# Kernel optimization log

Measured on AMD Instinct MI355X. Metric: run time of the kernel, lower is better.

## Reference

```python
import jax, jax.numpy as jnp
import numpy as np

TOP_K = 2

def setup_inputs() -> dict:
    key = jax.random.key(0)
    k1, k2 = jax.random.split(key)
    T, D, E = 16384, 2048, 64  # num_tokens, d_model, num_experts
    x = jax.random.normal(k1, (T, D), dtype=jnp.float32)
    Wg = jax.random.normal(k2, (D, E), dtype=jnp.float32) / np.sqrt(D)
    return {"x": x, "Wg": Wg}

def reference(x, Wg):
    T, E = x.shape[0], Wg.shape[1]
    # gate logits + softmax over experts
    logits = x @ Wg                                   # [T, E]
    probs = jax.nn.softmax(logits, axis=-1)           # [T, E]
    # top-k expert selection, renormalize selected weights
    top_vals, top_idx = jax.lax.top_k(probs, TOP_K)   # [T, K]
    top_vals = top_vals / jnp.sum(top_vals, axis=-1, keepdims=True)
    # scatter sparse gate weights into dense [T, E]
    rows = jnp.arange(T)[:, None]                     # [T, 1]
    gate_weights = jnp.zeros_like(probs).at[rows, top_idx].set(top_vals)
    # load-balance aux loss: E * sum_e f_e * P_e
    mask = jnp.sum(jax.nn.one_hot(top_idx, E, dtype=probs.dtype), axis=1)  # [T, E]
    f = jnp.mean(mask, axis=0)    # fraction of tokens routed to each expert
    P = jnp.mean(probs, axis=0)   # mean router prob per expert
    aux_loss = E * jnp.sum(f * P)
    return gate_weights, top_idx, aux_loss
```

## Files before the change

kernel.cpp:

```cpp
#include <hip/hip_runtime.h>


typedef __attribute__((ext_vector_type(8))) _Float16 half8;
typedef __attribute__((ext_vector_type(4))) float f32x4;

constexpr int DD  = 2048;
constexpr int EE  = 64;
constexpr int BM  = 16;
constexpr int BK  = 128;
constexpr int NCH = DD / BK;

#define WVM(N) asm volatile("s_waitcnt vmcnt(" #N ")" ::: "memory")
#define BAR()  asm volatile("s_barrier" ::: "memory")

__global__ __launch_bounds__(256) void wsplit_kernel(
    const float* __restrict__ Wg, _Float16* __restrict__ wF)
{
    __shared__ float xl[32][65];
    const int tid = threadIdx.x;
    const int kc  = blockIdx.x;
    const int k0  = kc * 32;
#pragma unroll
    for (int r = 0; r < 2; ++r) {
        int slot = tid + r * 256;
        int row = slot >> 4, c4 = (slot & 15) << 2;
        *(float4*)&xl[row][c4] = *(const float4*)&Wg[(size_t)(k0 + row) * EE + c4];
    }
    __syncthreads();
    const int t = tid >> 6, l = tid & 63;
    const int e  = t * 16 + (l & 15);
    const int kl = (l >> 4) * 8;
    half8 hh, ll;
#pragma unroll
    for (int j = 0; j < 8; ++j) {
        float v = xl[kl + j][e];
        _Float16 h = (_Float16)v;
        hh[j] = h;
        ll[j] = (_Float16)((v - (float)h) * 4096.f);
    }
    const size_t base = (size_t)(kc * 8 + t * 2) * 512 + (size_t)l * 8;
    *(half8*)&wF[base]       = hh;
    *(half8*)&wF[base + 512] = ll;
}

__global__ __launch_bounds__(256, 4) void gate_kernel(
    const float* __restrict__ x, const _Float16* __restrict__ wF,
    float* __restrict__ gate_out, float* __restrict__ idx_out,
    float* __restrict__ pSum, float* __restrict__ pCnt)
{
    __shared__ __align__(16) union {
        float xs[3][BM][BK];
        struct { float red[4][BM][68]; float auxsm[2][4][64]; } ep;
    } sm;

    const int tid  = threadIdx.x;
    const int kq   = tid >> 6;
    const int lane = tid & 63;
    const size_t tok0 = (size_t)blockIdx.x * BM;
    const float* xg = x + tok0 * DD;

    auto stageX = [&](int buf, int c) {
#pragma unroll
        for (int r = 0; r < 2; ++r) {
            int slot = tid + r * 256;
            int row  = slot >> 5;
            int cb   = (slot & 31) << 4;
            int sb   = cb ^ ((row & 7) << 5);
            __builtin_amdgcn_global_load_lds(
                xg + (size_t)row * DD + c * BK + (sb >> 2),
                &sm.xs[buf][row][cb >> 2], 16, 0, 0);
        }
    };

    f32x4 aH[4], aL[4];
#pragma unroll
    for (int t = 0; t < 4; ++t) {
        aH[t] = (f32x4){0.f, 0.f, 0.f, 0.f};
        aL[t] = (f32x4){0.f, 0.f, 0.f, 0.f};
    }

    const int rrow = lane & 15;
    const int rb   = (kq * 128 + ((lane >> 4) * 32)) ^ ((rrow & 7) << 5);

    auto compute = [&](int buf, int c) {
        const _Float16* wb = wF + (size_t)(c * 4 + kq) * 4096 + (size_t)lane * 8;
        half8 wh[4], wl[4];
#pragma unroll
        for (int t = 0; t < 4; ++t) {
            wh[t] = *(const half8*)(wb + (t * 2) * 512);
            wl[t] = *(const half8*)(wb + (t * 2 + 1) * 512);
        }
        const float* p = (const float*)((const char*)&sm.xs[buf][rrow][0] + rb);
        float4 xa = *(const float4*)p;
        float4 xb = *(const float4*)(p + 4);
        half8 ah, al;
        {
            float v;
            v = xa.x; { _Float16 h=(_Float16)v; ah[0]=h; al[0]=(_Float16)((v-(float)h)*4096.f); }
            v = xa.y; { _Float16 h=(_Float16)v; ah[1]=h; al[1]=(_Float16)((v-(float)h)*4096.f); }
            v = xa.z; { _Float16 h=(_Float16)v; ah[2]=h; al[2]=(_Float16)((v-(float)h)*4096.f); }
            v = xa.w; { _Float16 h=(_Float16)v; ah[3]=h; al[3]=(_Float16)((v-(float)h)*4096.f); }
            v = xb.x; { _Float16 h=(_Float16)v; ah[4]=h; al[4]=(_Float16)((v-(float)h)*4096.f); }
            v = xb.y; { _Float16 h=(_Float16)v; ah[5]=h; al[5]=(_Float16)((v-(float)h)*4096.f); }
            v = xb.z; { _Float16 h=(_Float16)v; ah[6]=h; al[6]=(_Float16)((v-(float)h)*4096.f); }
            v = xb.w; { _Float16 h=(_Float16)v; ah[7]=h; al[7]=(_Float16)((v-(float)h)*4096.f); }
        }
#pragma unroll
        for (int t = 0; t < 4; ++t) {
            aH[t] = __builtin_amdgcn_mfma_f32_16x16x32_f16(ah, wh[t], aH[t], 0, 0, 0);
            aL[t] = __builtin_amdgcn_mfma_f32_16x16x32_f16(ah, wl[t], aL[t], 0, 0, 0);
            aL[t] = __builtin_amdgcn_mfma_f32_16x16x32_f16(al, wh[t], aL[t], 0, 0, 0);
        }
    };

    stageX(0, 0);
    stageX(1, 1);

#pragma unroll 1
    for (int c = 0; c < NCH; ++c) {
        if (c < NCH - 1) { WVM(2); } else { WVM(0); }
        BAR();
        compute(c % 3, c);
        BAR();
        if (c + 2 < NCH) stageX((c + 2) % 3, c + 2);
    }

    __syncthreads();
    const float inv = 1.f / 4096.f;
#pragma unroll
    for (int e = 0; e < 4; ++e) {
        const int row = (lane >> 4) * 4 + e;
#pragma unroll
        for (int t = 0; t < 4; ++t)
            sm.ep.red[kq][row][t * 16 + (lane & 15)] = aH[t][e] + aL[t][e] * inv;
    }
    __syncthreads();

    float sumP_acc = 0.f;
    float cnt_acc  = 0.f;
#pragma unroll 1
    for (int tt = 0; tt < 4; ++tt) {
        const int tl = kq * 4 + tt;
        const size_t t = tok0 + tl;
        float v = (sm.ep.red[0][tl][lane] + sm.ep.red[1][tl][lane])
                + (sm.ep.red[2][tl][lane] + sm.ep.red[3][tl][lane]);

        float m = v;
#pragma unroll
        for (int off = 32; off; off >>= 1) m = fmaxf(m, __shfl_xor(m, off, 64));
        float p = expf(v - m);
        float s = p;
#pragma unroll
        for (int off = 32; off; off >>= 1) s += __shfl_xor(s, off, 64);
        float prob = p / s;
        sumP_acc += prob;

        float bv = prob; int bi = lane;
#pragma unroll
        for (int off = 32; off; off >>= 1) {
            float ov = __shfl_xor(bv, off, 64);
            int   oi = __shfl_xor(bi, off, 64);
            if (ov > bv || (ov == bv && oi < bi)) { bv = ov; bi = oi; }
        }
        float v2 = (lane == bi) ? -1.f : prob;
        float bv2 = v2; int bi2 = lane;
#pragma unroll
        for (int off = 32; off; off >>= 1) {
            float ov = __shfl_xor(bv2, off, 64);
            int   oi = __shfl_xor(bi2, off, 64);
            if (ov > bv2 || (ov == bv2 && oi < bi2)) { bv2 = ov; bi2 = oi; }
        }

        float denom = bv + bv2;
        float g1 = bv / denom, g2 = bv2 / denom;
        float g = (lane == bi) ? g1 : ((lane == bi2) ? g2 : 0.f);
        gate_out[t * EE + lane] = g;
        if (lane == 0) {
            idx_out[2 * t]     = (float)bi;
            idx_out[2 * t + 1] = (float)bi2;
        }
        cnt_acc += (lane == bi)  ? 1.f : 0.f;
        cnt_acc += (lane == bi2) ? 1.f : 0.f;
    }

    sm.ep.auxsm[0][kq][lane] = sumP_acc;
    sm.ep.auxsm[1][kq][lane] = cnt_acc;
    __syncthreads();
    if (kq == 0) {
        float sp = 0.f, c2 = 0.f;
#pragma unroll
        for (int w = 0; w < 4; ++w) {
            sp += sm.ep.auxsm[0][w][lane];
            c2 += sm.ep.auxsm[1][w][lane];
        }
        pSum[(size_t)blockIdx.x * 64 + lane] = sp;
        pCnt[(size_t)blockIdx.x * 64 + lane] = c2;
    }
}

__global__ __launch_bounds__(1024) void aux_kernel(
    const float* __restrict__ pSum, const float* __restrict__ pCnt,
    float* __restrict__ aux_out, int nblocks, float scale)
{
    const int tid  = threadIdx.x;
    const int wv   = tid >> 6;
    const int lane = tid & 63;
    __shared__ float smem[2][16][64];

    float sp[4] = {0.f, 0.f, 0.f, 0.f};
    float cc[4] = {0.f, 0.f, 0.f, 0.f};
    for (int b = wv * 4; b < nblocks; b += 64) {
#pragma unroll
        for (int u = 0; u < 4; ++u) {
            sp[u] += pSum[(size_t)(b + u) * 64 + lane];
            cc[u] += pCnt[(size_t)(b + u) * 64 + lane];
        }
    }
    smem[0][wv][lane] = (sp[0] + sp[1]) + (sp[2] + sp[3]);
    smem[1][wv][lane] = (cc[0] + cc[1]) + (cc[2] + cc[3]);
    __syncthreads();
    if (wv == 0) {
        float SP = 0.f, C = 0.f;
#pragma unroll
        for (int w = 0; w < 16; ++w) {
            SP += smem[0][w][lane];
            C  += smem[1][w][lane];
        }
        float prod = SP * C;
#pragma unroll
        for (int off = 32; off; off >>= 1) prod += __shfl_xor(prod, off, 64);
        if (lane == 0) aux_out[0] = prod * scale;
    }
}

extern "C" void kernel_launch(void* const* d_in, const int* in_sizes, int n_in,
                              void* d_out, int out_size, void* d_ws, size_t ws_size,
                              hipStream_t stream) {
    const float* x  = (const float*)d_in[0];
    const float* Wg = (const float*)d_in[1];
    const int T = in_sizes[0] / DD;

    float* out      = (float*)d_out;
    float* gate_out = out;
    float* idx_out  = out + (size_t)T * EE;
    float* aux_out  = idx_out + (size_t)T * 2;

    const int nblocks = T / BM;
    _Float16* wF = (_Float16*)d_ws;
    float* pSum = (float*)(wF + (size_t)64 * 8 * 512);
    float* pCnt = pSum + (size_t)nblocks * 64;

    wsplit_kernel<<<64, 256, 0, stream>>>(Wg, wF);
    gate_kernel<<<nblocks, 256, 0, stream>>>(x, wF, gate_out, idx_out, pSum, pCnt);

    const float scale = (float)EE / ((float)T * (float)T);
    aux_kernel<<<1, 1024, 0, stream>>>(pSum, pCnt, aux_out, nblocks, scale);
}
```

Before: 53.89 us.

## Deepen x staging to four buffers, prioritize MFMA, split aux reduction

Switches the x tile pipeline from three to four LDS buffers. Each chunk's load is now issued three chunks ahead, before the compute rather than after the trailing barrier, so more global loads are in flight while MFMAs run. It wraps the MFMA block in s_setprio to favour matrix issue. It also replaces the single-block aux reduction over 1024 partial rows with a 64-block first pass and a 1-block second pass, shortening the serial tail at the cost of one extra launch. The larger LDS footprint (32KB of x buffers) and the added launch may cut occupancy or add overhead. The second pass hardcodes 64 partial rows, so it assumes T=16384.

```diff
diff --git a/kernel.cpp b/kernel.cpp
--- a/kernel.cpp
+++ b/kernel.cpp
@@ -9,6 +9,7 @@
 constexpr int BM  = 16;
 constexpr int BK  = 128;
 constexpr int NCH = DD / BK;
+constexpr int NBUF = 4;
 
 #define WVM(N) asm volatile("s_waitcnt vmcnt(" #N ")" ::: "memory")
 #define BAR()  asm volatile("s_barrier" ::: "memory")
@@ -49,7 +50,7 @@
     float* __restrict__ pSum, float* __restrict__ pCnt)
 {
     __shared__ __align__(16) union {
-        float xs[3][BM][BK];
+        float xs[NBUF][BM][BK];
         struct { float red[4][BM][68]; float auxsm[2][4][64]; } ep;
     } sm;
 
@@ -105,24 +106,29 @@
             v = xb.z; { _Float16 h=(_Float16)v; ah[6]=h; al[6]=(_Float16)((v-(float)h)*4096.f); }
             v = xb.w; { _Float16 h=(_Float16)v; ah[7]=h; al[7]=(_Float16)((v-(float)h)*4096.f); }
         }
+        __builtin_amdgcn_s_setprio(1);
 #pragma unroll
         for (int t = 0; t < 4; ++t) {
             aH[t] = __builtin_amdgcn_mfma_f32_16x16x32_f16(ah, wh[t], aH[t], 0, 0, 0);
             aL[t] = __builtin_amdgcn_mfma_f32_16x16x32_f16(ah, wl[t], aL[t], 0, 0, 0);
             aL[t] = __builtin_amdgcn_mfma_f32_16x16x32_f16(al, wh[t], aL[t], 0, 0, 0);
         }
+        __builtin_amdgcn_s_setprio(0);
     };
 
     stageX(0, 0);
     stageX(1, 1);
+    stageX(2, 2);
 
 #pragma unroll 1
     for (int c = 0; c < NCH; ++c) {
-        if (c < NCH - 1) { WVM(2); } else { WVM(0); }
+        if (c < NCH - 2)       { WVM(4); }
+        else if (c == NCH - 2) { WVM(2); }
+        else                   { WVM(0); }
         BAR();
-        compute(c % 3, c);
+        if (c + 3 < NCH) stageX((c + 3) & 3, c + 3);
+        compute(c & 3, c);
         BAR();
-        if (c + 2 < NCH) stageX((c + 2) % 3, c + 2);
     }
 
     __syncthreads();
@@ -198,35 +204,59 @@
     }
 }
 
-__global__ __launch_bounds__(1024) void aux_kernel(
+__global__ __launch_bounds__(256) void aux1_kernel(
     const float* __restrict__ pSum, const float* __restrict__ pCnt,
-    float* __restrict__ aux_out, int nblocks, float scale)
+    float* __restrict__ p2Sum, float* __restrict__ p2Cnt)
 {
     const int tid  = threadIdx.x;
     const int wv   = tid >> 6;
     const int lane = tid & 63;
-    __shared__ float smem[2][16][64];
-
-    float sp[4] = {0.f, 0.f, 0.f, 0.f};
-    float cc[4] = {0.f, 0.f, 0.f, 0.f};
-    for (int b = wv * 4; b < nblocks; b += 64) {
-#pragma unroll
-        for (int u = 0; u < 4; ++u) {
-            sp[u] += pSum[(size_t)(b + u) * 64 + lane];
-            cc[u] += pCnt[(size_t)(b + u) * 64 + lane];
-        }
-    }
-    smem[0][wv][lane] = (sp[0] + sp[1]) + (sp[2] + sp[3]);
-    smem[1][wv][lane] = (cc[0] + cc[1]) + (cc[2] + cc[3]);
+    __shared__ float smem[2][4][64];
+
+    const int r0 = blockIdx.x * 16 + wv * 4;
+    float sp = 0.f, cc = 0.f;
+#pragma unroll
+    for (int u = 0; u < 4; ++u) {
+        sp += pSum[(size_t)(r0 + u) * 64 + lane];
+        cc += pCnt[(size_t)(r0 + u) * 64 + lane];
+    }
+    smem[0][wv][lane] = sp;
+    smem[1][wv][lane] = cc;
     __syncthreads();
     if (wv == 0) {
-        float SP = 0.f, C = 0.f;
-#pragma unroll
-        for (int w = 0; w < 16; ++w) {
-            SP += smem[0][w][lane];
-            C  += smem[1][w][lane];
-        }
-        float prod = SP * C;
+        float SP = smem[0][0][lane] + smem[0][1][lane]
+                 + smem[0][2][lane] + smem[0][3][lane];
+        float CC = smem[1][0][lane] + smem[1][1][lane]
+                 + smem[1][2][lane] + smem[1][3][lane];
+        p2Sum[(size_t)blockIdx.x * 64 + lane] = SP;
+        p2Cnt[(size_t)blockIdx.x * 64 + lane] = CC;
+    }
+}
+
+__global__ __launch_bounds__(256) void aux2_kernel(
+    const float* __restrict__ p2Sum, const float* __restrict__ p2Cnt,
+    float* __restrict__ aux_out, float scale)
+{
+    const int tid  = threadIdx.x;
+    const int wv   = tid >> 6;
+    const int lane = tid & 63;
+    __shared__ float smem[2][4][64];
+
+    float sp = 0.f, cc = 0.f;
+#pragma unroll 1
+    for (int b = wv * 16; b < wv * 16 + 16; ++b) {
+        sp += p2Sum[(size_t)b * 64 + lane];
+        cc += p2Cnt[(size_t)b * 64 + lane];
+    }
+    smem[0][wv][lane] = sp;
+    smem[1][wv][lane] = cc;
+    __syncthreads();
+    if (wv == 0) {
+        float SP = smem[0][0][lane] + smem[0][1][lane]
+                 + smem[0][2][lane] + smem[0][3][lane];
+        float CC = smem[1][0][lane] + smem[1][1][lane]
+                 + smem[1][2][lane] + smem[1][3][lane];
+        float prod = SP * CC;
 #pragma unroll
         for (int off = 32; off; off >>= 1) prod += __shfl_xor(prod, off, 64);
         if (lane == 0) aux_out[0] = prod * scale;
@@ -247,12 +277,15 @@
 
     const int nblocks = T / BM;
     _Float16* wF = (_Float16*)d_ws;
-    float* pSum = (float*)(wF + (size_t)64 * 8 * 512);
-    float* pCnt = pSum + (size_t)nblocks * 64;
+    float* pSum  = (float*)(wF + (size_t)64 * 8 * 512);
+    float* pCnt  = pSum + (size_t)nblocks * 64;
+    float* p2Sum = pCnt + (size_t)nblocks * 64;
+    float* p2Cnt = p2Sum + 64 * 64;
 
     wsplit_kernel<<<64, 256, 0, stream>>>(Wg, wF);
     gate_kernel<<<nblocks, 256, 0, stream>>>(x, wF, gate_out, idx_out, pSum, pCnt);
 
     const float scale = (float)EE / ((float)T * (float)T);
-    aux_kernel<<<1, 1024, 0, stream>>>(pSum, pCnt, aux_out, nblocks, scale);
-}
+    aux1_kernel<<<64, 256, 0, stream>>>(pSum, pCnt, p2Sum, p2Cnt);
+    aux2_kernel<<<1, 256, 0, stream>>>(p2Sum, p2Cnt, aux_out, scale);
+}
```

Result: slower. 58.94 us (+9.4%).
